# Kernel tuning notes

Hardware: AMD Instinct MI355X
Metric: run time of the kernel (lower is better)

## Reference

```python
import jax, jax.numpy as jnp
import numpy as np
from jax import lax

STRIDES = (8, 8, 16, 32, 32)
GRIDS = (40, 36, 24, 16, 12)
MIN_SCORE = 0.1
KEEP_SCORE = 0.1
MASK_THR = 0.5
UPDATE_THR = 0.05
SIGMA = 2.0
TOPN = 500
MAX_MASKS = 100
UP = 4


def points_nms(h):
    # max_pool2d(k=2, s=1, p=1) then crop last row/col == pad (1,0) window 2
    m = lax.reduce_window(h, -jnp.inf, lax.max, (1, 1, 2, 2), (1, 1, 1, 1),
                          ((0, 0), (0, 0), (1, 0), (1, 0)))
    return h * (m == h).astype(h.dtype)


def resize_mat(insz, outsz):
    # bilinear align_corners=True interpolation matrix [outsz, insz]
    if outsz > 1:
        src = jnp.arange(outsz, dtype=jnp.float32) * ((insz - 1) / (outsz - 1))
    else:
        src = jnp.zeros((outsz,), jnp.float32)
    lo = jnp.clip(jnp.floor(src).astype(jnp.int32), 0, insz - 1)
    hi = jnp.minimum(lo + 1, insz - 1)
    w = src - lo.astype(jnp.float32)
    r = jnp.arange(outsz)
    M = jnp.zeros((outsz, insz), jnp.float32)
    return M.at[r, lo].add(1.0 - w).at[r, hi].add(w)


def bilinear(x, oh, ow):  # x: [k,h,w]
    Mh = resize_mat(x.shape[1], oh)
    Mw = resize_mat(x.shape[2], ow)
    return jnp.einsum('Ww,kHw->kHW', Mw, jnp.einsum('Hh,khw->kHw', Mh, x))


def prep(cate_preds, kernel_preds):
    B = cate_preds[0].shape[0]
    cate = [points_nms(jax.nn.sigmoid(c)) for c in cate_preds]
    cate_flat = jnp.concatenate(
        [jnp.transpose(c, (0, 2, 3, 1)).reshape(B, -1, c.shape[1]) for c in cate], axis=1)
    kern_flat = jnp.concatenate(
        [jnp.transpose(k, (0, 2, 3, 1)).reshape(B, -1, k.shape[1]) for k in kernel_preds], axis=1)
    strides_vec = jnp.concatenate(
        [jnp.full((g * g,), float(s), jnp.float32) for g, s in zip(GRIDS, STRIDES)])
    return cate_flat, kern_flat, strides_vec


def decode_soft(mask_feat, cate_flat, kern_flat, strides_vec):
    # fixed-shape (padded) version of the per-image decode; invalid slots carry score 0
    nc = cate_flat.shape[-1]
    flat = cate_flat.reshape(-1)
    vals, idx = lax.top_k(jnp.where(flat > MIN_SCORE, flat, -1.0), TOPN)
    validk = vals > MIN_SCORE
    cell = idx // nc
    label = idx % nc
    # dynamic 1x1 conv == einsum with gathered kernels
    sig = jax.nn.sigmoid(jnp.einsum('kc,chw->khw', kern_flat[cell], mask_feat))
    binm = (sig > MASK_THR).astype(sig.dtype)
    summ = binm.sum((1, 2))
    keep = validk & (summ > strides_vec[cell])
    seg = (sig * binm).sum((1, 2)) / jnp.maximum(summ, 1e-6)
    scores = jnp.where(keep, vals * seg, 0.0)
    order = jnp.argsort(-scores)
    scores = scores[order]
    sig = sig[order]
    label = label[order]
    keep_o = keep[order]
    summ = jnp.where(keep, summ, 0.0)[order]
    binm = binm[order] * keep_o[:, None, None].astype(binm.dtype)
    # matrix NMS (gaussian)
    flatm = binm.reshape(TOPN, -1)
    inter = flatm @ flatm.T
    iou = inter / jnp.maximum(summ[:, None] + summ[None, :] - inter, 1e-6)
    triu = jnp.triu(jnp.ones((TOPN, TOPN), bool), 1)
    dmat = jnp.where(triu & (label[:, None] == label[None, :]), iou, 0.0)
    comp = dmat.max(0)  # max suppression each item received
    coef = (jnp.exp(-SIGMA * dmat**2) / jnp.exp(-SIGMA * comp[:, None]**2)).min(0)
    s2 = scores * coef
    s2 = jnp.where((s2 >= UPDATE_THR) & (s2 >= KEEP_SCORE) & keep_o, s2, 0.0)
    fv, fi = lax.top_k(s2, MAX_MASKS)
    return fv, jnp.where(fv > 0, label[fi], -1), sig[fi]


def reference(mask_feat_pred, cate_pred_0, cate_pred_1, cate_pred_2, cate_pred_3,
              cate_pred_4, kernel_pred_0, kernel_pred_1, kernel_pred_2, kernel_pred_3,
              kernel_pred_4, scaled_sizes, origin_sizes):
    cate_preds = [cate_pred_0, cate_pred_1, cate_pred_2, cate_pred_3, cate_pred_4]
    kernel_preds = [kernel_pred_0, kernel_pred_1, kernel_pred_2, kernel_pred_3, kernel_pred_4]
    cate_flat, kern_flat, sv = prep(cate_preds, kernel_preds)
    fv, lab, sig = jax.vmap(lambda mf, cf, kf: decode_soft(mf, cf, kf, sv))(
        mask_feat_pred, cate_flat, kern_flat)
    H = mask_feat_pred.shape[2] * UP
    W = mask_feat_pred.shape[3] * UP
    up = jax.vmap(lambda s: bilinear(s, H, W))(sig)  # [B,M,H,W]
    sh, sw = int(scaled_sizes[0, 0]), int(scaled_sizes[0, 1])
    oh, ow = int(origin_sizes[0, 0]), int(origin_sizes[0, 1])
    up = up[:, :, :sh, :sw]
    up = jax.vmap(lambda s: bilinear(s, oh, ow))(up)
    masks = ((up > MASK_THR) & (fv > 0)[:, :, None, None]).astype(jnp.uint8)
    return masks, lab, fv


def setup_inputs() -> dict:
    key = jax.random.key(0)
    ks = jax.random.split(key, 11)
    B, C, NC, HM = 2, 256, 80, 128
    inp = {'mask_feat_pred': jax.random.normal(ks[0], (B, C, HM, HM), jnp.float32)}
    for i, g in enumerate(GRIDS):
        inp[f'cate_pred_{i}'] = jax.random.normal(ks[1 + i], (B, NC, g, g), jnp.float32)
        inp[f'kernel_pred_{i}'] = jax.random.normal(ks[6 + i], (B, C, g, g), jnp.float32) * 0.05
    inp['scaled_sizes'] = jnp.full((B, 2), HM * UP, jnp.int32)
    inp['origin_sizes'] = jnp.full((B, 2), HM * UP, jnp.int32)
    return inp
```

## Files before the change

kernel.cpp:

```cpp
#include <hip/hip_runtime.h>
#include <math.h>
#include <stdint.h>

#define NBATCH 2
#define NC 80
#define CHN 256
#define HMM 128
#define HWN (HMM*HMM)
#define NCELL 3872
#define FLATN (NCELL*NC)
#define TOPN 500
#define SROWS 512
#define MAXM 100
#define OUTH 512
#define OUTW 512
#define NBINS 1024
#define CANDCAP 1024
#define BM 128
#define BN 128
#define BK 16
#define GNB (HWN/BN)

__device__ __forceinline__ float sigmoidf_(float x){ return 1.0f/(1.0f+expf(-x)); }

__device__ __forceinline__ void cell_decode(int cell, int& lvl, int& g, int& y, int& x){
  int off;
  if (cell < 1600)      { lvl=0; g=40; off=0; }
  else if (cell < 2896) { lvl=1; g=36; off=1600; }
  else if (cell < 3472) { lvl=2; g=24; off=2896; }
  else if (cell < 3728) { lvl=3; g=16; off=3472; }
  else                  { lvl=4; g=12; off=3728; }
  int r = cell - off; y = r / g; x = r - y*g;
}

template<int N, int NT>
__device__ __forceinline__ void bitonic_desc(uint64_t* key){
  int tid = threadIdx.x;
  for (int k = 2; k <= N; k <<= 1)
    for (int j = k >> 1; j > 0; j >>= 1) {
      __syncthreads();
      for (int e = tid; e < N; e += NT) {
        int l = e ^ j;
        if (l > e) {
          uint64_t a = key[e], c = key[l];
          bool up = ((e & k) == 0);
          if (up ? (a < c) : (a > c)) { key[e] = c; key[l] = a; }
        }
      }
    }
  __syncthreads();
}

__global__ void k1_scores(const float* __restrict__ c0, const float* __restrict__ c1,
                          const float* __restrict__ c2, const float* __restrict__ c3,
                          const float* __restrict__ c4,
                          float* __restrict__ scores_t, uint32_t* __restrict__ hist){
  int t = blockIdx.x*blockDim.x + threadIdx.x;
  if (t >= NBATCH*FLATN) return;
  int b = t / FLATN;
  int rem = t - b*FLATN;
  int c = rem / NCELL;
  int cell = rem - c*NCELL;
  int lvl,g,y,x; cell_decode(cell,lvl,g,y,x);
  const float* cp = lvl==0?c0:lvl==1?c1:lvl==2?c2:lvl==3?c3:c4;
  const float* base = cp + (size_t)(b*NC + c)*g*g;
  float raw = base[y*g + x];
  float m = raw;
  if (y > 0)          m = fmaxf(m, base[(y-1)*g + x]);
  if (x > 0)          m = fmaxf(m, base[y*g + x-1]);
  if (y > 0 && x > 0) m = fmaxf(m, base[(y-1)*g + x-1]);
  float s = (raw == m) ? sigmoidf_(raw) : 0.0f;
  scores_t[t] = s;
  if (s > 0.1f) {
    int bin = (int)(s * 1024.0f); if (bin > NBINS-1) bin = NBINS-1;
    atomicAdd(&hist[b*NBINS + bin], 1u);
  }
}

__global__ __launch_bounds__(1024) void k2_cutoff(const uint32_t* __restrict__ hist, int* __restrict__ cutoff){
  __shared__ uint32_t h[NBINS];
  int b = blockIdx.x;
  h[threadIdx.x] = hist[b*NBINS + threadIdx.x];
  __syncthreads();
  if (threadIdx.x == 0) {
    int acc = 0; int cut = 0;
    for (int d = NBINS-1; d >= 0; --d) {
      acc += (int)h[d];
      if (acc >= TOPN) { cut = d; break; }
    }
    cutoff[b] = cut;
  }
}

__global__ void k3_gather(const float* __restrict__ scores_t, const int* __restrict__ cutoff,
                          uint32_t* __restrict__ cnt, float* __restrict__ cval, uint32_t* __restrict__ cidx){
  int t = blockIdx.x*blockDim.x + threadIdx.x;
  if (t >= NBATCH*FLATN) return;
  int b = t / FLATN;
  int rem = t - b*FLATN;
  int c = rem / NCELL;
  int cell = rem - c*NCELL;
  float v = scores_t[t];
  if (v > 0.1f) {
    int bin = (int)(v * 1024.0f); if (bin > NBINS-1) bin = NBINS-1;
    if (bin >= cutoff[b]) {
      uint32_t p = atomicAdd(&cnt[b], 1u);
      if (p < CANDCAP) { cval[b*CANDCAP+p] = v; cidx[b*CANDCAP+p] = (uint32_t)(cell*NC + c); }
    }
  }
}

__global__ __launch_bounds__(512) void k4_sort(const uint32_t* __restrict__ cnt,
        const float* __restrict__ cval, const uint32_t* __restrict__ cidx,
        float* __restrict__ vals, int* __restrict__ cellA, int* __restrict__ labelA){
  __shared__ uint64_t key[CANDCAP];
  int b = blockIdx.x; int tid = threadIdx.x;
  int n = (int)cnt[b]; if (n > CANDCAP) n = CANDCAP;
  for (int e = tid; e < CANDCAP; e += 512) {
    uint64_t k = 0;
    if (e < n)
      k = ((uint64_t)__float_as_uint(cval[b*CANDCAP+e]) << 32) |
          (uint64_t)(0xFFFFFFFFu - cidx[b*CANDCAP+e]);
    key[e] = k;
  }
  bitonic_desc<CANDCAP,512>(key);
  for (int r = tid; r < TOPN; r += 512) {
    uint64_t k = key[r];
    if ((k >> 32) == 0) { vals[b*TOPN+r] = -1.0f; cellA[b*TOPN+r] = 0; labelA[b*TOPN+r] = 0; }
    else {
      uint32_t idx = 0xFFFFFFFFu - (uint32_t)(k & 0xFFFFFFFFu);
      vals[b*TOPN+r]   = __uint_as_float((uint32_t)(k >> 32));
      cellA[b*TOPN+r]  = (int)(idx / NC);
      labelA[b*TOPN+r] = (int)(idx % NC);
    }
  }
}

__global__ void k5_kmat(const float* __restrict__ k0p, const float* __restrict__ k1p,
                        const float* __restrict__ k2p, const float* __restrict__ k3p,
                        const float* __restrict__ k4p,
                        const int* __restrict__ cellA, float* __restrict__ Kmat){
  int t = blockIdx.x*blockDim.x + threadIdx.x;
  if (t >= NBATCH*TOPN*CHN) return;
  int b = t / (TOPN*CHN); int rem = t - b*(TOPN*CHN);
  int k = rem / CHN; int c = rem - k*CHN;
  int cell = cellA[b*TOPN + k];
  int lvl,g,y,x; cell_decode(cell,lvl,g,y,x);
  const float* kp = lvl==0?k0p:lvl==1?k1p:lvl==2?k2p:lvl==3?k3p:k4p;
  Kmat[t] = kp[((size_t)(b*CHN + c)*g + y)*g + x];
}

__global__ __launch_bounds__(256) void k6_gemm1(const float* __restrict__ Kmat, const float* __restrict__ mf,
        float* __restrict__ sigfull, uint32_t* __restrict__ bits,
        float* __restrict__ psum, float* __restrict__ pseg){
  __shared__ alignas(16) float As[BK][BM+4];
  __shared__ alignas(16) float Bs[BK][BN];
  int tid = threadIdx.x;
  int nb = blockIdx.x, mb = blockIdx.y, b = blockIdx.z;
  int row0 = mb*BM, col0 = nb*BN;
  int tx = tid & 15, ty = tid >> 4;

  int ar[2], aq[2], bkk[2], bcc[2];
  #pragma unroll
  for (int i = 0; i < 2; ++i) {
    int e = i*256 + tid;
    ar[i] = e >> 2; aq[i] = e & 3;
    bkk[i] = e >> 5; bcc[i] = e & 31;
  }
  float4 pa[2], pb[2];
  const float4 z4 = make_float4(0.f,0.f,0.f,0.f);
  #pragma unroll
  for (int i = 0; i < 2; ++i) {
    int rr = row0 + ar[i];
    pa[i] = (rr < TOPN) ? *(const float4*)&Kmat[((size_t)b*TOPN + rr)*CHN + aq[i]*4] : z4;
  }
  #pragma unroll
  for (int i = 0; i < 2; ++i)
    pb[i] = *(const float4*)&mf[((size_t)b*CHN + bkk[i])*HWN + col0 + bcc[i]*4];

  float acc[8][8];
  #pragma unroll
  for (int i=0;i<8;i++)
    #pragma unroll
    for(int j=0;j<8;j++) acc[i][j]=0.f;

  for (int k0 = 0; k0 < CHN; k0 += BK) {
    __syncthreads();
    #pragma unroll
    for (int i = 0; i < 2; ++i) {
      int colA = ar[i] ^ (aq[i] << 2);
      As[aq[i]*4+0][colA] = pa[i].x;
      As[aq[i]*4+1][colA] = pa[i].y;
      As[aq[i]*4+2][colA] = pa[i].z;
      As[aq[i]*4+3][colA] = pa[i].w;
    }
    #pragma unroll
    for (int i = 0; i < 2; ++i)
      *(float4*)&Bs[bkk[i]][bcc[i]*4] = pb[i];
    __syncthreads();
    if (k0 + BK < CHN) {
      int k0n = k0 + BK;
      #pragma unroll
      for (int i = 0; i < 2; ++i) {
        int rr = row0 + ar[i];
        pa[i] = (rr < TOPN) ? *(const float4*)&Kmat[((size_t)b*TOPN + rr)*CHN + k0n + aq[i]*4] : z4;
      }
      #pragma unroll
      for (int i = 0; i < 2; ++i)
        pb[i] = *(const float4*)&mf[((size_t)b*CHN + k0n + bkk[i])*HWN + col0 + bcc[i]*4];
    }
    #pragma unroll 4
    for (int kk = 0; kk < BK; ++kk) {
      int s = (kk >> 2) << 2;
      float4 a0 = *(float4*)&As[kk][(ty*8) ^ s];
      float4 a1 = *(float4*)&As[kk][(ty*8+4) ^ s];
      float4 b0 = *(float4*)&Bs[kk][tx*4];
      float4 b1 = *(float4*)&Bs[kk][64+tx*4];
      float av[8] = {a0.x,a0.y,a0.z,a0.w,a1.x,a1.y,a1.z,a1.w};
      #pragma unroll
      for (int i = 0; i < 8; ++i) {
        acc[i][0] += av[i]*b0.x; acc[i][1] += av[i]*b0.y; acc[i][2] += av[i]*b0.z; acc[i][3] += av[i]*b0.w;
        acc[i][4] += av[i]*b1.x; acc[i][5] += av[i]*b1.y; acc[i][6] += av[i]*b1.z; acc[i][7] += av[i]*b1.w;
      }
    }
  }
  #pragma unroll
  for (int i = 0; i < 8; ++i) {
    int r = row0 + ty*8 + i;
    float se = 0.f; int cc = 0;
    #pragma unroll
    for (int q = 0; q < 2; ++q) {
      float4 sv;
      sv.x = sigmoidf_(acc[i][q*4+0]);
      sv.y = sigmoidf_(acc[i][q*4+1]);
      sv.z = sigmoidf_(acc[i][q*4+2]);
      sv.w = sigmoidf_(acc[i][q*4+3]);
      uint32_t m = 0;
      if (sv.x > 0.5f) { m |= 1u; se += sv.x; cc++; }
      if (sv.y > 0.5f) { m |= 2u; se += sv.y; cc++; }
      if (sv.z > 0.5f) { m |= 4u; se += sv.z; cc++; }
      if (sv.w > 0.5f) { m |= 8u; se += sv.w; cc++; }
      uint32_t wrd = m << ((tx & 7)*4);
      wrd |= __shfl_xor(wrd, 1);
      wrd |= __shfl_xor(wrd, 2);
      wrd |= __shfl_xor(wrd, 4);
      if ((tx & 7) == 0 && r < TOPN)
        bits[((size_t)b*TOPN + r)*512 + nb*4 + q*2 + (tx>>3)] = wrd;
      *(float4*)&sigfull[((size_t)b*SROWS + r)*HWN + col0 + q*64 + tx*4] = sv;
    }
    #pragma unroll
    for (int d = 1; d < 16; d <<= 1) {
      se += __shfl_xor(se, d);
      cc += __shfl_xor(cc, d);
    }
    if (tx == 0 && r < TOPN) {
      psum[((size_t)b*TOPN + r)*GNB + nb] = (float)cc;
      pseg[((size_t)b*TOPN + r)*GNB + nb] = se;
    }
  }
}

__global__ __launch_bounds__(512) void k78_stats_order(const float* __restrict__ psum, const float* __restrict__ pseg,
        const float* __restrict__ vals, const int* __restrict__ cellA,
        float* __restrict__ summ, float* __restrict__ scores, int* __restrict__ keepA,
        int* __restrict__ order){
  __shared__ uint64_t key[512];
  int b = blockIdx.x, tid = threadIdx.x;
  uint64_t k = 0;
  if (tid < TOPN) {
    int t = b*TOPN + tid;
    float sc = 0.f, sg = 0.f;
    for (int i = 0; i < GNB; i += 4) {
      float4 a = *(const float4*)&psum[(size_t)t*GNB+i];
      float4 c = *(const float4*)&pseg[(size_t)t*GNB+i];
      sc += a.x+a.y+a.z+a.w; sg += c.x+c.y+c.z+c.w;
    }
    float v = vals[t];
    int cell = cellA[t];
    int lvl,g,y,x; cell_decode(cell,lvl,g,y,x);
    float stride = (lvl<=1)?8.f:(lvl==2)?16.f:32.f;
    bool keep = (v > 0.1f) && (sc > stride);
    float seg = sg / fmaxf(sc, 1e-6f);
    summ[t] = sc;
    float s = keep ? v*seg : 0.f;
    scores[t] = s;
    keepA[t] = keep ? 1 : 0;
    k = ((uint64_t)__float_as_uint(s) << 32) | (uint64_t)(0xFFFFFFFFu - (uint32_t)tid);
  }
  key[tid] = k;
  bitonic_desc<512,512>(key);
  if (tid < TOPN) order[b*TOPN+tid] = (int)(0xFFFFFFFFu - (uint32_t)(key[tid] & 0xFFFFFFFFu));
}

__global__ __launch_bounds__(256) void k9_dmat(const uint32_t* __restrict__ bitsG,
        const int* __restrict__ order, const int* __restrict__ labelA, const int* __restrict__ keepA,
        const float* __restrict__ summ, float* __restrict__ dmatT){
  __shared__ uint32_t rowb[512];
  int i = blockIdx.x, b = blockIdx.y, tid = threadIdx.x;
  int oi = order[b*TOPN + i];
  if (!keepA[b*TOPN + oi]) return;
  float si = summ[b*TOPN + oi];
  int li = labelA[b*TOPN + oi];
  for (int w = tid; w < 512; w += 256) rowb[w] = bitsG[((size_t)b*TOPN + oi)*512 + w];
  __syncthreads();
  for (int j = i + 1 + tid; j < TOPN; j += 256) {
    int oj = order[b*TOPN + j];
    if (!keepA[b*TOPN + oj] || labelA[b*TOPN + oj] != li) continue;
    const uint4* rj = (const uint4*)&bitsG[((size_t)b*TOPN + oj)*512];
    const uint4* ri = (const uint4*)rowb;
    int cc = 0;
    for (int w = 0; w < 128; ++w) {
      uint4 x = rj[w], y = ri[w];
      cc += __popc(x.x & y.x) + __popc(x.y & y.y) + __popc(x.z & y.z) + __popc(x.w & y.w);
    }
    float sj = summ[b*TOPN + oj];
    float inter = (float)cc;
    dmatT[((size_t)b*TOPN + j)*TOPN + i] = inter / fmaxf(si + sj - inter, 1e-6f);
  }
}

__global__ __launch_bounds__(256) void k10_comp(const float* __restrict__ dmatT,
        float* __restrict__ comp, float* __restrict__ e2c){
  __shared__ float red[4];
  int j = blockIdx.x, b = blockIdx.y, tid = threadIdx.x;
  float m = 0.f;
  for (int i = tid; i < TOPN; i += 256) m = fmaxf(m, dmatT[((size_t)b*TOPN+j)*TOPN + i]);
  #pragma unroll
  for (int d = 1; d < 64; d <<= 1) m = fmaxf(m, __shfl_xor(m, d));
  if ((tid & 63) == 0) red[tid >> 6] = m;
  __syncthreads();
  if (tid == 0) {
    m = fmaxf(fmaxf(red[0], red[1]), fmaxf(red[2], red[3]));
    comp[b*TOPN+j] = m;
    e2c[b*TOPN+j] = expf(-2.0f*m*m);
  }
}

__global__ __launch_bounds__(256) void k10_coef(const float* __restrict__ dmatT, const float* __restrict__ e2c,
        const float* __restrict__ scores, const int* __restrict__ order, const int* __restrict__ keepA,
        float* __restrict__ s2){
  __shared__ float red[4];
  int j = blockIdx.x, b = blockIdx.y, tid = threadIdx.x;
  float mn = 1e30f;
  for (int i = tid; i < TOPN; i += 256) {
    float d = dmatT[((size_t)b*TOPN+j)*TOPN + i];
    float r = expf(-2.0f*d*d) / e2c[b*TOPN+i];
    mn = fminf(mn, r);
  }
  #pragma unroll
  for (int d = 1; d < 64; d <<= 1) mn = fminf(mn, __shfl_xor(mn, d));
  if ((tid & 63) == 0) red[tid >> 6] = mn;
  __syncthreads();
  if (tid == 0) {
    mn = fminf(fminf(red[0], red[1]), fminf(red[2], red[3]));
    int oj = order[b*TOPN+j];
    float s = scores[b*TOPN+oj] * mn;
    bool ok = (s >= 0.05f) && (s >= 0.1f) && (keepA[b*TOPN+oj] != 0);
    s2[b*TOPN+j] = ok ? s : 0.f;
  }
}

__global__ __launch_bounds__(512) void k11_top100(const float* __restrict__ s2, const int* __restrict__ order,
        const int* __restrict__ labelA, float* __restrict__ outF, int* __restrict__ selrow){
  __shared__ uint64_t key[512];
  int b = blockIdx.x, tid = threadIdx.x;
  uint64_t k = 0;
  if (tid < TOPN)
    k = ((uint64_t)__float_as_uint(s2[b*TOPN+tid]) << 32) | (uint64_t)(0xFFFFFFFFu - (uint32_t)tid);
  key[tid] = k;
  bitonic_desc<512,512>(key);
  if (tid < MAXM) {
    uint64_t kk = key[tid];
    float v = __uint_as_float((uint32_t)(kk >> 32));
    int j = (int)(0xFFFFFFFFu - (uint32_t)(kk & 0xFFFFFFFFu));
    if (j < 0 || j >= TOPN) { j = 0; v = 0.f; }
    int orow = order[b*TOPN + j];
    float lab = (v > 0.f) ? (float)labelA[b*TOPN + orow] : -1.0f;
    size_t maskCount = (size_t)NBATCH*MAXM*OUTH*OUTW;
    outF[maskCount + (size_t)b*MAXM + tid] = lab;
    outF[maskCount + (size_t)NBATCH*MAXM + (size_t)b*MAXM + tid] = v;
    selrow[b*MAXM + tid] = orow;
  }
}

__global__ void k13_upsample(const float* __restrict__ sigfull, const int* __restrict__ selrow,
                             float* __restrict__ outF){
  int t = blockIdx.x*blockDim.x + threadIdx.x;
  const int XG = OUTW/4;
  int total = NBATCH*MAXM*OUTH*XG;
  if (t >= total) return;
  int xg = t % XG;
  int tmp = t / XG;
  int Y = tmp % OUTH;
  int tmp2 = tmp / OUTH;
  int r = tmp2 % MAXM;
  int b = tmp2 / MAXM;
  size_t maskCount = (size_t)NBATCH*MAXM*OUTH*OUTW;
  float fv = outF[maskCount + (size_t)NBATCH*MAXM + (size_t)b*MAXM + r];
  float4 o = make_float4(0.f,0.f,0.f,0.f);
  if (fv > 0.f) {
    const float* sm = sigfull + ((size_t)b*SROWS + selrow[b*MAXM + r])*HWN;
    const float SC = (float)(127.0/511.0);
    float fy = (float)Y * SC;
    int ly = (int)floorf(fy); if (ly < 0) ly = 0; if (ly > HMM-1) ly = HMM-1;
    int hy = ly+1 < HMM ? ly+1 : HMM-1;
    float wy = fy - (float)ly;
    float res[4];
    #pragma unroll
    for (int u = 0; u < 4; ++u) {
      int X = xg*4 + u;
      float fx = (float)X * SC;
      int lx = (int)floorf(fx); if (lx < 0) lx = 0; if (lx > HMM-1) lx = HMM-1;
      int hx = lx+1 < HMM ? lx+1 : HMM-1;
      float wx = fx - (float)lx;
      float a = (1.f-wy)*sm[ly*HMM+lx] + wy*sm[hy*HMM+lx];
      float c = (1.f-wy)*sm[ly*HMM+hx] + wy*sm[hy*HMM+hx];
      float v = (1.f-wx)*a + wx*c;
      res[u] = (v > 0.5f) ? 1.f : 0.f;
    }
    o = make_float4(res[0],res[1],res[2],res[3]);
  }
  *(float4*)&outF[(((size_t)b*MAXM + r)*OUTH + Y)*OUTW + xg*4] = o;
}

extern "C" void kernel_launch(void* const* d_in, const int* in_sizes, int n_in,
                              void* d_out, int out_size, void* d_ws, size_t ws_size,
                              hipStream_t stream) {
  const float* mf = (const float*)d_in[0];
  const float *cate[5], *kern[5];
  bool interleaved = (n_in > 2) && (in_sizes[2] == NBATCH*CHN*40*40);
  if (interleaved) {
    for (int i = 0; i < 5; ++i) { cate[i] = (const float*)d_in[1 + 2*i]; kern[i] = (const float*)d_in[2 + 2*i]; }
  } else {
    for (int i = 0; i < 5; ++i) { cate[i] = (const float*)d_in[1 + i]; kern[i] = (const float*)d_in[6 + i]; }
  }
  float* outF = (float*)d_out;

  uint8_t* p = (uint8_t*)d_ws;
  auto alloc = [&](size_t bytes) -> void* {
    void* r = (void*)p;
    p += (bytes + 255) & ~(size_t)255;
    return r;
  };
  float*    scores_t    = (float*)   alloc((size_t)NBATCH*FLATN*4);
  uint32_t* hist        = (uint32_t*)alloc((size_t)(NBATCH*NBINS + NBATCH)*4);
  uint32_t* cnt         = hist + NBATCH*NBINS;
  int*      cutoff      = (int*)     alloc((size_t)NBATCH*4);
  float*    cval        = (float*)   alloc((size_t)NBATCH*CANDCAP*4);
  uint32_t* cidx        = (uint32_t*)alloc((size_t)NBATCH*CANDCAP*4);
  float*    vals        = (float*)   alloc((size_t)NBATCH*TOPN*4);
  int*      cellA       = (int*)     alloc((size_t)NBATCH*TOPN*4);
  int*      labelA      = (int*)     alloc((size_t)NBATCH*TOPN*4);
  float*    Kmat        = (float*)   alloc((size_t)NBATCH*TOPN*CHN*4);
  uint32_t* bits        = (uint32_t*)alloc((size_t)NBATCH*TOPN*512*4);
  float*    psum        = (float*)   alloc((size_t)NBATCH*TOPN*GNB*4);
  float*    pseg        = (float*)   alloc((size_t)NBATCH*TOPN*GNB*4);
  float*    summ        = (float*)   alloc((size_t)NBATCH*TOPN*4);
  float*    scores      = (float*)   alloc((size_t)NBATCH*TOPN*4);
  int*      keepA       = (int*)     alloc((size_t)NBATCH*TOPN*4);
  int*      order       = (int*)     alloc((size_t)NBATCH*TOPN*4);
  float*    dmatT       = (float*)   alloc((size_t)NBATCH*TOPN*TOPN*4);
  float*    comp        = (float*)   alloc((size_t)NBATCH*TOPN*4);
  float*    e2c         = (float*)   alloc((size_t)NBATCH*TOPN*4);
  float*    s2          = (float*)   alloc((size_t)NBATCH*TOPN*4);
  int*      selrow      = (int*)     alloc((size_t)NBATCH*MAXM*4);
  float*    sigfull     = (float*)   alloc((size_t)NBATCH*SROWS*HWN*4);
  (void)ws_size; (void)out_size;

  hipMemsetAsync(hist, 0, (size_t)(NBATCH*NBINS + NBATCH)*4, stream);
  hipMemsetAsync(dmatT, 0, (size_t)NBATCH*TOPN*TOPN*4, stream);
  hipLaunchKernelGGL(k1_scores, dim3((NBATCH*FLATN + 255)/256), dim3(256), 0, stream,
                     cate[0], cate[1], cate[2], cate[3], cate[4], scores_t, hist);
  hipLaunchKernelGGL(k2_cutoff, dim3(NBATCH), dim3(1024), 0, stream, hist, cutoff);
  hipLaunchKernelGGL(k3_gather, dim3((NBATCH*FLATN + 255)/256), dim3(256), 0, stream,
                     scores_t, cutoff, cnt, cval, cidx);
  hipLaunchKernelGGL(k4_sort, dim3(NBATCH), dim3(512), 0, stream, cnt, cval, cidx, vals, cellA, labelA);
  hipLaunchKernelGGL(k5_kmat, dim3((NBATCH*TOPN*CHN + 255)/256), dim3(256), 0, stream,
                     kern[0], kern[1], kern[2], kern[3], kern[4], cellA, Kmat);
  hipLaunchKernelGGL(k6_gemm1, dim3(GNB, (TOPN+BM-1)/BM, NBATCH), dim3(256), 0, stream,
                     Kmat, mf, sigfull, bits, psum, pseg);
  hipLaunchKernelGGL(k78_stats_order, dim3(NBATCH), dim3(512), 0, stream,
                     psum, pseg, vals, cellA, summ, scores, keepA, order);
  hipLaunchKernelGGL(k9_dmat, dim3(TOPN, NBATCH), dim3(256), 0, stream,
                     bits, order, labelA, keepA, summ, dmatT);
  hipLaunchKernelGGL(k10_comp, dim3(TOPN, NBATCH), dim3(256), 0, stream, dmatT, comp, e2c);
  hipLaunchKernelGGL(k10_coef, dim3(TOPN, NBATCH), dim3(256), 0, stream,
                     dmatT, e2c, scores, order, keepA, s2);
  hipLaunchKernelGGL(k11_top100, dim3(NBATCH), dim3(512), 0, stream, s2, order, labelA, outF, selrow);
  hipLaunchKernelGGL(k13_upsample, dim3((NBATCH*MAXM*OUTH*(OUTW/4) + 255)/256), dim3(256), 0, stream,
                     sigfull, selrow, outF);
}
```

Measured before the change: 384.9 us.

## Double-buffer GEMM shared tiles, fuse column-max into dmat, trim bitonic barriers

The mask GEMM now keeps two shared-memory buffers, so each K-step needs one barrier instead of two and the next tile is written while the current one is consumed. The separate k10_comp kernel is removed: k9_dmat folds the per-column IoU max into comp with atomicMax on the float bit pattern, and k78 zeroes comp first. k10_coef recomputes exp(-2c^2) inline. The bitonic sort skips barriers for strides under 32, relying on wavefront-synchronous execution. This is only safe on 64-wide wavefronts and only with a memory fence between LDS accesses, so it risks correctness. The doubled LDS and the atomics may reduce occupancy or add contention.

```diff
diff --git a/kernel.cpp b/kernel.cpp
--- a/kernel.cpp
+++ b/kernel.cpp
@@ -36,9 +36,10 @@
 template<int N, int NT>
 __device__ __forceinline__ void bitonic_desc(uint64_t* key){
   int tid = threadIdx.x;
+  __syncthreads();
   for (int k = 2; k <= N; k <<= 1)
     for (int j = k >> 1; j > 0; j >>= 1) {
-      __syncthreads();
+      if (j >= 32) __syncthreads();
       for (int e = tid; e < N; e += NT) {
         int l = e ^ j;
         if (l > e) {
@@ -153,8 +154,8 @@
 __global__ __launch_bounds__(256) void k6_gemm1(const float* __restrict__ Kmat, const float* __restrict__ mf,
         float* __restrict__ sigfull, uint32_t* __restrict__ bits,
         float* __restrict__ psum, float* __restrict__ pseg){
-  __shared__ alignas(16) float As[BK][BM+4];
-  __shared__ alignas(16) float Bs[BK][BN];
+  __shared__ alignas(16) float As[2][BK][BM+4];
+  __shared__ alignas(16) float Bs[2][BK][BN];
   int tid = threadIdx.x;
   int nb = blockIdx.x, mb = blockIdx.y, b = blockIdx.z;
   int row0 = mb*BM, col0 = nb*BN;
@@ -173,10 +174,18 @@
   for (int i = 0; i < 2; ++i) {
     int rr = row0 + ar[i];
     pa[i] = (rr < TOPN) ? *(const float4*)&Kmat[((size_t)b*TOPN + rr)*CHN + aq[i]*4] : z4;
-  }
-  #pragma unroll
-  for (int i = 0; i < 2; ++i)
     pb[i] = *(const float4*)&mf[((size_t)b*CHN + bkk[i])*HWN + col0 + bcc[i]*4];
+  }
+  #pragma unroll
+  for (int i = 0; i < 2; ++i) {
+    int colA = ar[i] ^ (aq[i] << 2);
+    As[0][aq[i]*4+0][colA] = pa[i].x;
+    As[0][aq[i]*4+1][colA] = pa[i].y;
+    As[0][aq[i]*4+2][colA] = pa[i].z;
+    As[0][aq[i]*4+3][colA] = pa[i].w;
+    *(float4*)&Bs[0][bkk[i]][bcc[i]*4] = pb[i];
+  }
+  __syncthreads();
 
   float acc[8][8];
   #pragma unroll
@@ -184,44 +193,45 @@
     #pragma unroll
     for(int j=0;j<8;j++) acc[i][j]=0.f;
 
+  int cur = 0;
   for (int k0 = 0; k0 < CHN; k0 += BK) {
-    __syncthreads();
-    #pragma unroll
-    for (int i = 0; i < 2; ++i) {
-      int colA = ar[i] ^ (aq[i] << 2);
-      As[aq[i]*4+0][colA] = pa[i].x;
-      As[aq[i]*4+1][colA] = pa[i].y;
-      As[aq[i]*4+2][colA] = pa[i].z;
-      As[aq[i]*4+3][colA] = pa[i].w;
-    }
-    #pragma unroll
-    for (int i = 0; i < 2; ++i)
-      *(float4*)&Bs[bkk[i]][bcc[i]*4] = pb[i];
-    __syncthreads();
-    if (k0 + BK < CHN) {
+    bool more = (k0 + BK < CHN);
+    if (more) {
       int k0n = k0 + BK;
       #pragma unroll
       for (int i = 0; i < 2; ++i) {
         int rr = row0 + ar[i];
         pa[i] = (rr < TOPN) ? *(const float4*)&Kmat[((size_t)b*TOPN + rr)*CHN + k0n + aq[i]*4] : z4;
+        pb[i] = *(const float4*)&mf[((size_t)b*CHN + k0n + bkk[i])*HWN + col0 + bcc[i]*4];
       }
-      #pragma unroll
-      for (int i = 0; i < 2; ++i)
-        pb[i] = *(const float4*)&mf[((size_t)b*CHN + k0n + bkk[i])*HWN + col0 + bcc[i]*4];
     }
     #pragma unroll 4
     for (int kk = 0; kk < BK; ++kk) {
       int s = (kk >> 2) << 2;
-      float4 a0 = *(float4*)&As[kk][(ty*8) ^ s];
-      float4 a1 = *(float4*)&As[kk][(ty*8+4) ^ s];
-      float4 b0 = *(float4*)&Bs[kk][tx*4];
-      float4 b1 = *(float4*)&Bs[kk][64+tx*4];
+      float4 a0 = *(float4*)&As[cur][kk][(ty*8) ^ s];
+      float4 a1 = *(float4*)&As[cur][kk][(ty*8+4) ^ s];
+      float4 b0 = *(float4*)&Bs[cur][kk][tx*4];
+      float4 b1 = *(float4*)&Bs[cur][kk][64+tx*4];
       float av[8] = {a0.x,a0.y,a0.z,a0.w,a1.x,a1.y,a1.z,a1.w};
       #pragma unroll
       for (int i = 0; i < 8; ++i) {
         acc[i][0] += av[i]*b0.x; acc[i][1] += av[i]*b0.y; acc[i][2] += av[i]*b0.z; acc[i][3] += av[i]*b0.w;
         acc[i][4] += av[i]*b1.x; acc[i][5] += av[i]*b1.y; acc[i][6] += av[i]*b1.z; acc[i][7] += av[i]*b1.w;
       }
+    }
+    if (more) {
+      int nxt = cur ^ 1;
+      #pragma unroll
+      for (int i = 0; i < 2; ++i) {
+        int colA = ar[i] ^ (aq[i] << 2);
+        As[nxt][aq[i]*4+0][colA] = pa[i].x;
+        As[nxt][aq[i]*4+1][colA] = pa[i].y;
+        As[nxt][aq[i]*4+2][colA] = pa[i].z;
+        As[nxt][aq[i]*4+3][colA] = pa[i].w;
+        *(float4*)&Bs[nxt][bkk[i]][bcc[i]*4] = pb[i];
+      }
+      __syncthreads();
+      cur = nxt;
     }
   }
   #pragma unroll
@@ -263,12 +273,13 @@
 __global__ __launch_bounds__(512) void k78_stats_order(const float* __restrict__ psum, const float* __restrict__ pseg,
         const float* __restrict__ vals, const int* __restrict__ cellA,
         float* __restrict__ summ, float* __restrict__ scores, int* __restrict__ keepA,
-        int* __restrict__ order){
+        int* __restrict__ order, float* __restrict__ comp){
   __shared__ uint64_t key[512];
   int b = blockIdx.x, tid = threadIdx.x;
   uint64_t k = 0;
   if (tid < TOPN) {
     int t = b*TOPN + tid;
+    comp[t] = 0.f;
     float sc = 0.f, sg = 0.f;
     for (int i = 0; i < GNB; i += 4) {
       float4 a = *(const float4*)&psum[(size_t)t*GNB+i];
@@ -294,7 +305,7 @@
 
 __global__ __launch_bounds__(256) void k9_dmat(const uint32_t* __restrict__ bitsG,
         const int* __restrict__ order, const int* __restrict__ labelA, const int* __restrict__ keepA,
-        const float* __restrict__ summ, float* __restrict__ dmatT){
+        const float* __restrict__ summ, float* __restrict__ dmatT, float* __restrict__ comp){
   __shared__ uint32_t rowb[512];
   int i = blockIdx.x, b = blockIdx.y, tid = threadIdx.x;
   int oi = order[b*TOPN + i];
@@ -315,28 +326,13 @@
     }
     float sj = summ[b*TOPN + oj];
     float inter = (float)cc;
-    dmatT[((size_t)b*TOPN + j)*TOPN + i] = inter / fmaxf(si + sj - inter, 1e-6f);
-  }
-}
-
-__global__ __launch_bounds__(256) void k10_comp(const float* __restrict__ dmatT,
-        float* __restrict__ comp, float* __restrict__ e2c){
-  __shared__ float red[4];
-  int j = blockIdx.x, b = blockIdx.y, tid = threadIdx.x;
-  float m = 0.f;
-  for (int i = tid; i < TOPN; i += 256) m = fmaxf(m, dmatT[((size_t)b*TOPN+j)*TOPN + i]);
-  #pragma unroll
-  for (int d = 1; d < 64; d <<= 1) m = fmaxf(m, __shfl_xor(m, d));
-  if ((tid & 63) == 0) red[tid >> 6] = m;
-  __syncthreads();
-  if (tid == 0) {
-    m = fmaxf(fmaxf(red[0], red[1]), fmaxf(red[2], red[3]));
-    comp[b*TOPN+j] = m;
-    e2c[b*TOPN+j] = expf(-2.0f*m*m);
-  }
-}
-
-__global__ __launch_bounds__(256) void k10_coef(const float* __restrict__ dmatT, const float* __restrict__ e2c,
+    float v = inter / fmaxf(si + sj - inter, 1e-6f);
+    dmatT[((size_t)b*TOPN + j)*TOPN + i] = v;
+    if (v > 0.f) atomicMax((int*)&comp[b*TOPN + j], __float_as_int(v));
+  }
+}
+
+__global__ __launch_bounds__(256) void k10_coef(const float* __restrict__ dmatT, const float* __restrict__ comp,
         const float* __restrict__ scores, const int* __restrict__ order, const int* __restrict__ keepA,
         float* __restrict__ s2){
   __shared__ float red[4];
@@ -344,7 +340,8 @@
   float mn = 1e30f;
   for (int i = tid; i < TOPN; i += 256) {
     float d = dmatT[((size_t)b*TOPN+j)*TOPN + i];
-    float r = expf(-2.0f*d*d) / e2c[b*TOPN+i];
+    float c = comp[b*TOPN+i];
+    float r = expf(-2.0f*d*d) / expf(-2.0f*c*c);
     mn = fminf(mn, r);
   }
   #pragma unroll
@@ -461,7 +458,6 @@
   int*      order       = (int*)     alloc((size_t)NBATCH*TOPN*4);
   float*    dmatT       = (float*)   alloc((size_t)NBATCH*TOPN*TOPN*4);
   float*    comp        = (float*)   alloc((size_t)NBATCH*TOPN*4);
-  float*    e2c         = (float*)   alloc((size_t)NBATCH*TOPN*4);
   float*    s2          = (float*)   alloc((size_t)NBATCH*TOPN*4);
   int*      selrow      = (int*)     alloc((size_t)NBATCH*MAXM*4);
   float*    sigfull     = (float*)   alloc((size_t)NBATCH*SROWS*HWN*4);
@@ -480,12 +476,11 @@
   hipLaunchKernelGGL(k6_gemm1, dim3(GNB, (TOPN+BM-1)/BM, NBATCH), dim3(256), 0, stream,
                      Kmat, mf, sigfull, bits, psum, pseg);
   hipLaunchKernelGGL(k78_stats_order, dim3(NBATCH), dim3(512), 0, stream,
-                     psum, pseg, vals, cellA, summ, scores, keepA, order);
+                     psum, pseg, vals, cellA, summ, scores, keepA, order, comp);
   hipLaunchKernelGGL(k9_dmat, dim3(TOPN, NBATCH), dim3(256), 0, stream,
-                     bits, order, labelA, keepA, summ, dmatT);
-  hipLaunchKernelGGL(k10_comp, dim3(TOPN, NBATCH), dim3(256), 0, stream, dmatT, comp, e2c);
+                     bits, order, labelA, keepA, summ, dmatT, comp);
   hipLaunchKernelGGL(k10_coef, dim3(TOPN, NBATCH), dim3(256), 0, stream,
-                     dmatT, e2c, scores, order, keepA, s2);
+                     dmatT, comp, scores, order, keepA, s2);
   hipLaunchKernelGGL(k11_top100, dim3(NBATCH), dim3(512), 0, stream, s2, order, labelA, outF, selrow);
   hipLaunchKernelGGL(k13_upsample, dim3((NBATCH*MAXM*OUTH*(OUTW/4) + 255)/256), dim3(256), 0, stream,
                      sigfull, selrow, outF);
```

Result: no change. 385.7 us (+0.2%).
